# Performance work log

Hardware: AMD Instinct MI355X
Metric: run time of the kernel (lower is better)

The kernel has to match this reference:

```python
import jax, jax.numpy as jnp
import numpy as np


def _normalize(x):
    # channel mean-subtract then channel L2 normalize, as in MIDMs.forward
    x = x - x.mean(axis=1, keepdims=True)
    return x / jnp.linalg.norm(x, axis=1, keepdims=True)


def setup_inputs() -> dict:
    key = jax.random.key(0)
    ks = jax.random.split(key, 6)
    B, C, H, W = 2, 256, 64, 64
    return {
        "trg_out": jax.random.normal(ks[0], (B, C, H, W), jnp.float32),
        "src_out": jax.random.normal(ks[1], (B, C, H, W), jnp.float32),
        "ref_out": jax.random.normal(ks[2], (B, C, H, W), jnp.float32),
        "src_feats": jax.random.normal(ks[3], (B, 4, H, W), jnp.float32),
        "ref_feats": jax.random.normal(ks[4], (B, 4, H, W), jnp.float32),
        "ref_semantics": jax.random.uniform(ks[5], (B, 151, H, W), jnp.float32),
    }


def reference(trg_out, src_out, ref_out, src_feats, ref_feats, ref_semantics):
    B, C, H, W = trg_out.shape
    L = H * W
    # normalized matching features, flattened over spatial positions
    t = _normalize(trg_out).reshape(B, C, L)   # [B, C, Lt]
    s = _normalize(src_out).reshape(B, C, L)   # [B, C, Ls]
    r = _normalize(ref_out).reshape(B, C, L)

    # Correlation.correlation: dense cosine affinity between all position pairs
    corr_src = jnp.einsum("bci,bcj->bij", t, s)  # [B, Lt, Ls]
    corr_ref = jnp.einsum("bci,bcj->bij", t, r)

    # soft_warp: softmax over source positions, attention-weighted gather
    attn_src = jax.nn.softmax(corr_src, axis=-1)
    attn_ref = jax.nn.softmax(corr_ref, axis=-1)

    warped_src_feat = jnp.einsum("bij,bcj->bci", attn_src,
                                 src_feats.reshape(B, -1, L)).reshape(B, -1, H, W)
    warped_ref_feat = jnp.einsum("bij,bcj->bci", attn_ref,
                                 ref_feats.reshape(B, -1, L)).reshape(B, -1, H, W)
    warped_ref_seg = jnp.einsum("bij,bcj->bci", attn_ref,
                                ref_semantics.reshape(B, -1, L)).reshape(B, -1, H, W)
    return warped_src_feat, warped_ref_feat, warped_ref_seg
```

## Files before the change

kernel.cpp:

```cpp
#include <hip/hip_runtime.h>
#include <hip/hip_bf16.h>
#include <cstdint>
#include <cstddef>

typedef unsigned short u16;
typedef __attribute__((ext_vector_type(8))) __bf16 bf16x8;
typedef __attribute__((ext_vector_type(4))) unsigned u32x4;
typedef __attribute__((ext_vector_type(16))) float f32x16;

#define LPOS 4096
#define CDIM 256
#define LDSBUF 13312

#if __has_builtin(__builtin_amdgcn_exp2f)
#define EXP2(x) __builtin_amdgcn_exp2f(x)
#else
#define EXP2(x) exp2f(x)
#endif

#define GLOAD_LDS16(g, l)                                                      \
  __builtin_amdgcn_global_load_lds(                                            \
      (const __attribute__((address_space(1))) void*)(g),                      \
      (__attribute__((address_space(3))) void*)(l), 16, 0, 0)

__device__ __forceinline__ unsigned f2bfbits(float x) {
  union { float f; unsigned u; } v; v.f = x;
  return (v.u + 0x7FFFu + ((v.u >> 16) & 1u)) >> 16;
}
__device__ __forceinline__ unsigned packbf(float a, float b) {
  __hip_bfloat162 h2 = __float22bfloat162_rn(make_float2(a, b));
  return *(unsigned*)&h2;
}

__global__ void norm_fused(const float* __restrict__ t_in,
                           const float* __restrict__ s_in,
                           const float* __restrict__ r_in,
                           u16* __restrict__ qn, u16* __restrict__ ksn,
                           u16* __restrict__ krn) {
  __shared__ float tile[256 * 33];
  __shared__ float sums[256], sqs[256];
  __shared__ float mv[32], ivv[32];
  int idx = blockIdx.x;
  int ab = idx >> 7, lt = idx & 127;
  int arr = ab >> 1, b = ab & 1;
  int l0 = lt * 32;
  const float* inp = (arr == 0 ? t_in : arr == 1 ? s_in : r_in) + (size_t)b * CDIM * LPOS;
  u16* outp = (arr == 0 ? qn : arr == 1 ? ksn : krn) + (size_t)b * LPOS * CDIM;
  float scale = (arr == 0) ? 1.4426950408889634f : 1.0f;
  int t = threadIdx.x;
  int cg = t >> 5, l = t & 31;
  float sum = 0.f, sq = 0.f;
#pragma unroll 8
  for (int cc = 0; cc < 32; ++cc) {
    int c = cg * 32 + cc;
    float v = inp[(size_t)c * LPOS + l0 + l];
    tile[c * 33 + l] = v;
    sum += v; sq += v * v;
  }
  sums[t] = sum; sqs[t] = sq;
  __syncthreads();
  if (t < 32) {
    float s = 0.f, q = 0.f;
#pragma unroll
    for (int g = 0; g < 8; ++g) { s += sums[g * 32 + t]; q += sqs[g * 32 + t]; }
    float mean = s * (1.0f / CDIM);
    float nsq = q - s * s * (1.0f / CDIM);
    mv[t] = mean;
    ivv[t] = rsqrtf(fmaxf(nsq, 1e-20f)) * scale;
  }
  __syncthreads();
  int c2 = t & 127, ph = t >> 7;
#pragma unroll 4
  for (int rr = 0; rr < 16; ++rr) {
    int pos = ph + rr * 2;
    float m = mv[pos], iv = ivv[pos];
    float v0 = (tile[(2 * c2) * 33 + pos] - m) * iv;
    float v1 = (tile[(2 * c2 + 1) * 33 + pos] - m) * iv;
    *(unsigned*)&outp[(size_t)(l0 + pos) * CDIM + 2 * c2] = packbf(v0, v1);
  }
}

__global__ void build_v(const float* __restrict__ sf, const float* __restrict__ rf,
                        const float* __restrict__ sem,
                        u16* __restrict__ vs, u16* __restrict__ vr) {
  int t = blockIdx.x * 256 + threadIdx.x;
  const int NVS = 2 * 32 * 4096;
  if (t < NVS) {
    int b = t >> 17;
    int c = (t >> 12) & 31;
    int j = t & 4095;
    float v = (c < 4) ? sf[((size_t)b * 4 + c) * LPOS + j] : (c == 4 ? 1.0f : 0.0f);
    vs[t] = (u16)f2bfbits(v);
  } else {
    int t2 = t - NVS;
    if (t2 < 2 * 160 * 4096) {
      int b = t2 / (160 * 4096);
      int rr = t2 % (160 * 4096);
      int c = rr >> 12, j = rr & 4095;
      float v = (c < 151) ? sem[((size_t)b * 151 + c) * LPOS + j]
              : (c < 155) ? rf[((size_t)b * 4 + (c - 151)) * LPOS + j]
              : (c == 155) ? 1.0f : 0.0f;
      vr[((size_t)b * 160 + c) * LPOS + j] = (u16)f2bfbits(v);
    }
  }
}

template <int CT>
__device__ __forceinline__ void flash_body(
    const u16* __restrict__ qb, const u16* __restrict__ kb,
    const u16* __restrict__ vb, float* __restrict__ dst,
    u16 (*lds)[LDSBUF], int wave, int lane, int i_wave, int j_base, int iters) {
  int h = lane >> 5, ln = lane & 31;

  bf16x8 qf[16];
  const u16* qrow = qb + (size_t)(i_wave + ln) * CDIM;
#pragma unroll
  for (int kt = 0; kt < 16; ++kt)
    qf[kt] = *(const bf16x8*)(qrow + kt * 16 + h * 8);
#pragma unroll
  for (int kt = 0; kt < 16; ++kt)
    asm volatile("" : "+v"(*(u32x4*)&qf[kt]));

  f32x16 O[CT];
#pragma unroll
  for (int c = 0; c < CT; ++c)
#pragma unroll
    for (int t = 0; t < 16; ++t) O[c][t] = 0.0f;

  auto stage = [&](int j0s, int buf) {
#pragma unroll
    for (int g = 0; g < 4; ++g) {
      int G = wave * 4 + g;
      int j = 2 * G + h;
      GLOAD_LDS16(kb + (size_t)(j0s + j) * CDIM + (ln ^ (j & 7)) * 8,
                  &lds[buf][G * 512]);
    }
    if constexpr (CT == 5) {
#pragma unroll
      for (int g = 0; g < 3; ++g) {
        int s = wave + g * 4;
        if (s < 10) {
          int f = s * 64 + lane;
          int p = f / 160;
          int c = f - p * 160;
          GLOAD_LDS16(vb + (size_t)c * LPOS + j0s + p * 8,
                      &lds[buf][8192 + s * 512]);
        }
      }
    }
  };

  int kread_base = ln * 256 + 8 * (h ^ (ln & 1));
  int q = (ln >> 1) & 3;
  const u16* ka[4];
#pragma unroll
  for (int m = 0; m < 4; ++m) ka[m] = &lds[0][kread_base + 16 * (m ^ q)];
  const u16* va = &lds[0][8192 + h * 1280 + ln * 8];

  stage(j_base, 0);
  if (iters > 1) stage(j_base + 32, 1);

  int buf = 0;
  for (int jt = 0; jt < iters; ++jt) {
    int j0 = j_base + jt * 32;
    int bo = buf * LDSBUF;

    if (jt == iters - 1) {
      asm volatile("s_waitcnt vmcnt(0)" ::: "memory");
    } else if (CT == 5) {
      asm volatile("s_waitcnt vmcnt(6)" ::: "memory");
    } else {
      asm volatile("s_waitcnt vmcnt(4)" ::: "memory");
    }
    __builtin_amdgcn_sched_barrier(0);
    __builtin_amdgcn_s_barrier();
    __builtin_amdgcn_sched_barrier(0);

    bf16x8 vf[2];
    if constexpr (CT == 1) {
#pragma unroll
      for (int kt2 = 0; kt2 < 2; ++kt2)
        vf[kt2] = *(const bf16x8*)(vb + (size_t)ln * LPOS + j0 + (2 * kt2 + h) * 8);
    }
    if (jt + 2 < iters) {
      int b2 = buf ? buf - 1 : 2;
      stage(j0 + 64, b2);
    }

    __builtin_amdgcn_s_setprio(1);

    f32x16 Sa, Sb;
#pragma unroll
    for (int t = 0; t < 16; ++t) { Sa[t] = 0.0f; Sb[t] = 0.0f; }
#pragma unroll
    for (int kt = 0; kt < 16; kt += 2) {
      bf16x8 ka0 = *(const bf16x8*)(ka[kt & 3] + 64 * (kt >> 2) + bo);
      Sa = __builtin_amdgcn_mfma_f32_32x32x16_bf16(ka0, qf[kt], Sa, 0, 0, 0);
      bf16x8 ka1 = *(const bf16x8*)(ka[(kt + 1) & 3] + 64 * ((kt + 1) >> 2) + bo);
      Sb = __builtin_amdgcn_mfma_f32_32x32x16_bf16(ka1, qf[kt + 1], Sb, 0, 0, 0);
    }
    f32x16 S;
#pragma unroll
    for (int t = 0; t < 16; ++t) S[t] = EXP2(Sa[t] + Sb[t]);

    bf16x8 pb[2];
#pragma unroll
    for (int kh = 0; kh < 2; ++kh) {
      unsigned c0 = packbf(S[kh * 8 + 0], S[kh * 8 + 1]);
      unsigned c1 = packbf(S[kh * 8 + 2], S[kh * 8 + 3]);
      unsigned c2 = packbf(S[kh * 8 + 4], S[kh * 8 + 5]);
      unsigned c3 = packbf(S[kh * 8 + 6], S[kh * 8 + 7]);
      asm("v_permlane32_swap_b32 %0, %1" : "+v"(c0), "+v"(c2));
      asm("v_permlane32_swap_b32 %0, %1" : "+v"(c1), "+v"(c3));
      union { unsigned u[4]; bf16x8 v; } tmp;
      tmp.u[0] = c0;
      tmp.u[1] = c1;
      tmp.u[2] = c2;
      tmp.u[3] = c3;
      pb[kh] = tmp.v;
    }

#pragma unroll
    for (int ct = 0; ct < CT; ++ct)
#pragma unroll
      for (int kt2 = 0; kt2 < 2; ++kt2) {
        bf16x8 vax;
        if constexpr (CT == 5)
          vax = *(const bf16x8*)(va + kt2 * 2560 + ct * 256 + bo);
        else
          vax = vf[kt2];
        O[ct] = __builtin_amdgcn_mfma_f32_32x32x16_bf16(vax, pb[kt2], O[ct], 0, 0, 0);
      }

    __builtin_amdgcn_s_setprio(0);

    buf = (buf == 2) ? 0 : buf + 1;
  }

  const int climit = (CT == 1) ? 5 : 156;
#pragma unroll
  for (int ct = 0; ct < CT; ++ct)
#pragma unroll
    for (int t = 0; t < 16; ++t) {
      int c = ct * 32 + (t & 3) + 8 * (t >> 2) + 4 * h;
      if (c < climit)
        dst[(size_t)c * LPOS + i_wave + ln] = O[ct][t];
    }
}

__global__ __launch_bounds__(256, 2) void flash(
    const u16* __restrict__ qn, const u16* __restrict__ ksn, const u16* __restrict__ krn,
    const u16* __restrict__ vs, const u16* __restrict__ vr,
    float* __restrict__ nsrc, float* __restrict__ nref,
    int nch_src, int nch_ref) {
  __shared__ u16 lds[3][LDSBUF];
  int tid = threadIdx.x;
  int wave = tid >> 6, lane = tid & 63;
  int idx = blockIdx.x;
  int nrefb = 64 * nch_ref;
  if (idx < nrefb) {
    int r = idx;
    int chunk = r >> 6, b = (r >> 5) & 1, wgi = r & 31;
    int jchunk = LPOS / nch_ref;
    flash_body<5>(qn + (size_t)b * LPOS * CDIM, krn + (size_t)b * LPOS * CDIM,
                  vr + (size_t)b * 160 * LPOS,
                  nref + (size_t)(chunk * 2 + b) * 160 * LPOS,
                  lds, wave, lane, wgi * 128 + wave * 32, chunk * jchunk,
                  jchunk / 32);
  } else {
    int r = idx - nrefb;
    int chunk = r >> 6, b = (r >> 5) & 1, wgi = r & 31;
    int jchunk = LPOS / nch_src;
    flash_body<1>(qn + (size_t)b * LPOS * CDIM, ksn + (size_t)b * LPOS * CDIM,
                  vs + (size_t)b * 32 * LPOS,
                  nsrc + (size_t)(chunk * 2 + b) * 32 * LPOS,
                  lds, wave, lane, wgi * 128 + wave * 32, chunk * jchunk,
                  jchunk / 32);
  }
}

__global__ void finalize(const float* __restrict__ nsrc, const float* __restrict__ nref,
                         float* __restrict__ out, int nch_src, int nch_ref) {
  int v = blockIdx.x * 256 + threadIdx.x;
  if (v >= 325632) return;
  float nx = 0.f, ny = 0.f, nz = 0.f, nw = 0.f;
  float dx = 0.f, dy = 0.f, dz = 0.f, dw = 0.f;
  if (v < 8192) {
    int b = v >> 12, c = (v >> 10) & 3, i4 = v & 1023;
    for (int k = 0; k < nch_src; ++k) {
      const float* base = nsrc + ((size_t)(k * 2 + b) * 32) * LPOS;
      float4 n4 = ((const float4*)(base + (size_t)c * LPOS))[i4];
      float4 d4 = ((const float4*)(base + (size_t)4 * LPOS))[i4];
      nx += n4.x; ny += n4.y; nz += n4.z; nw += n4.w;
      dx += d4.x; dy += d4.y; dz += d4.z; dw += d4.w;
    }
  } else if (v < 16384) {
    int v1 = v - 8192;
    int b = v1 >> 12, c = (v1 >> 10) & 3, i4 = v1 & 1023;
    for (int k = 0; k < nch_ref; ++k) {
      const float* base = nref + ((size_t)(k * 2 + b) * 160) * LPOS;
      float4 n4 = ((const float4*)(base + (size_t)(151 + c) * LPOS))[i4];
      float4 d4 = ((const float4*)(base + (size_t)155 * LPOS))[i4];
      nx += n4.x; ny += n4.y; nz += n4.z; nw += n4.w;
      dx += d4.x; dy += d4.y; dz += d4.z; dw += d4.w;
    }
  } else {
    int v2 = v - 16384;
    int b = v2 / 154624;
    int rr = v2 - b * 154624;
    int c = rr >> 10, i4 = rr & 1023;
    for (int k = 0; k < nch_ref; ++k) {
      const float* base = nref + ((size_t)(k * 2 + b) * 160) * LPOS;
      float4 n4 = ((const float4*)(base + (size_t)c * LPOS))[i4];
      float4 d4 = ((const float4*)(base + (size_t)155 * LPOS))[i4];
      nx += n4.x; ny += n4.y; nz += n4.z; nw += n4.w;
      dx += d4.x; dy += d4.y; dz += d4.z; dw += d4.w;
    }
  }
  float4 r;
  r.x = nx / dx; r.y = ny / dy; r.z = nz / dz; r.w = nw / dw;
  ((float4*)out)[v] = r;
}

extern "C" void kernel_launch(void* const* d_in, const int* in_sizes, int n_in,
                              void* d_out, int out_size, void* d_ws, size_t ws_size,
                              hipStream_t stream) {
  const float* trg  = (const float*)d_in[0];
  const float* srcp = (const float*)d_in[1];
  const float* refp = (const float*)d_in[2];
  const float* sfeat = (const float*)d_in[3];
  const float* rfeat = (const float*)d_in[4];
  const float* rsem  = (const float*)d_in[5];
  float* out = (float*)d_out;

  char* ws = (char*)d_ws;
  size_t o = 0;
  auto alloc = [&](size_t bytes) -> char* {
    char* p = ws + o;
    o += (bytes + 255) & ~(size_t)255;
    return p;
  };
  u16* qn  = (u16*)alloc(2ull * LPOS * CDIM * 2);
  u16* ksn = (u16*)alloc(2ull * LPOS * CDIM * 2);
  u16* krn = (u16*)alloc(2ull * LPOS * CDIM * 2);
  u16* vs  = (u16*)alloc(2ull * 32 * LPOS * 2);
  u16* vr  = (u16*)alloc(2ull * 160 * LPOS * 2);

  size_t fixed = o;
  int nch_ref = 8;
  for (;;) {
    size_t need = fixed + 512 +
                  (size_t)nch_ref * 2 * 32 * LPOS * 4 +
                  (size_t)nch_ref * 2 * 160 * LPOS * 4;
    if (need <= ws_size || nch_ref == 1) break;
    nch_ref >>= 1;
  }
  int nch_src = nch_ref;
  float* nsrc = (float*)alloc((size_t)nch_src * 2 * 32 * LPOS * 4);
  float* nref = (float*)alloc((size_t)nch_ref * 2 * 160 * LPOS * 4);

  hipLaunchKernelGGL(norm_fused, dim3(768), dim3(256), 0, stream,
                     trg, srcp, refp, qn, ksn, krn);
  hipLaunchKernelGGL(build_v, dim3(6144), dim3(256), 0, stream,
                     sfeat, rfeat, rsem, vs, vr);
  hipLaunchKernelGGL(flash, dim3(64 * (nch_ref + nch_src)), dim3(256), 0, stream,
                     qn, ksn, krn, vs, vr, nsrc, nref, nch_src, nch_ref);
  hipLaunchKernelGGL(finalize, dim3(1272), dim3(256), 0, stream,
                     nsrc, nref, out, nch_src, nch_ref);
}
```

Baseline: 147.1 us.

## Software-pipeline QK MFMA with previous tile's exp and PV accumulation

Restructures the main loop so that each iteration computes the QK scores for the current tile, then runs exp, bf16 packing and the PV MFMAs for the previous tile, with a drain step after the loop. The goal is to hide the exp/transcendental latency and the dependency stalls between score and output MFMAs by interleaving independent work. It also drops the prefetch distance from two tiles ahead to one and waits for all outstanding loads (vmcnt(0)) each iteration, which may expose global load latency. The carried score accumulator adds register pressure.

```diff
diff --git a/kernel.cpp b/kernel.cpp
--- a/kernel.cpp
+++ b/kernel.cpp
@@ -157,52 +157,14 @@
   for (int m = 0; m < 4; ++m) ka[m] = &lds[0][kread_base + 16 * (m ^ q)];
   const u16* va = &lds[0][8192 + h * 1280 + ln * 8];
 
-  stage(j_base, 0);
-  if (iters > 1) stage(j_base + 32, 1);
-
-  int buf = 0;
-  for (int jt = 0; jt < iters; ++jt) {
-    int j0 = j_base + jt * 32;
-    int bo = buf * LDSBUF;
-
-    if (jt == iters - 1) {
-      asm volatile("s_waitcnt vmcnt(0)" ::: "memory");
-    } else if (CT == 5) {
-      asm volatile("s_waitcnt vmcnt(6)" ::: "memory");
-    } else {
-      asm volatile("s_waitcnt vmcnt(4)" ::: "memory");
-    }
-    __builtin_amdgcn_sched_barrier(0);
-    __builtin_amdgcn_s_barrier();
-    __builtin_amdgcn_sched_barrier(0);
-
-    bf16x8 vf[2];
-    if constexpr (CT == 1) {
-#pragma unroll
-      for (int kt2 = 0; kt2 < 2; ++kt2)
-        vf[kt2] = *(const bf16x8*)(vb + (size_t)ln * LPOS + j0 + (2 * kt2 + h) * 8);
-    }
-    if (jt + 2 < iters) {
-      int b2 = buf ? buf - 1 : 2;
-      stage(j0 + 64, b2);
-    }
-
-    __builtin_amdgcn_s_setprio(1);
-
-    f32x16 Sa, Sb;
-#pragma unroll
-    for (int t = 0; t < 16; ++t) { Sa[t] = 0.0f; Sb[t] = 0.0f; }
-#pragma unroll
-    for (int kt = 0; kt < 16; kt += 2) {
-      bf16x8 ka0 = *(const bf16x8*)(ka[kt & 3] + 64 * (kt >> 2) + bo);
-      Sa = __builtin_amdgcn_mfma_f32_32x32x16_bf16(ka0, qf[kt], Sa, 0, 0, 0);
-      bf16x8 ka1 = *(const bf16x8*)(ka[(kt + 1) & 3] + 64 * ((kt + 1) >> 2) + bo);
-      Sb = __builtin_amdgcn_mfma_f32_32x32x16_bf16(ka1, qf[kt + 1], Sb, 0, 0, 0);
-    }
+  f32x16 Sp;
+#pragma unroll
+  for (int t = 0; t < 16; ++t) Sp[t] = 0.0f;
+
+  auto finish_prev = [&](int pbo, const bf16x8* vfp) {
     f32x16 S;
 #pragma unroll
-    for (int t = 0; t < 16; ++t) S[t] = EXP2(Sa[t] + Sb[t]);
-
+    for (int t = 0; t < 16; ++t) S[t] = EXP2(Sp[t]);
     bf16x8 pb[2];
 #pragma unroll
     for (int kh = 0; kh < 2; ++kh) {
@@ -219,22 +181,75 @@
       tmp.u[3] = c3;
       pb[kh] = tmp.v;
     }
-
 #pragma unroll
     for (int ct = 0; ct < CT; ++ct)
 #pragma unroll
       for (int kt2 = 0; kt2 < 2; ++kt2) {
         bf16x8 vax;
         if constexpr (CT == 5)
-          vax = *(const bf16x8*)(va + kt2 * 2560 + ct * 256 + bo);
+          vax = *(const bf16x8*)(va + kt2 * 2560 + ct * 256 + pbo);
         else
-          vax = vf[kt2];
+          vax = vfp[kt2];
         O[ct] = __builtin_amdgcn_mfma_f32_32x32x16_bf16(vax, pb[kt2], O[ct], 0, 0, 0);
       }
+  };
+
+  stage(j_base, 0);
+
+  int buf = 0, pbo = 0;
+  for (int jt = 0; jt < iters; ++jt) {
+    int j0 = j_base + jt * 32;
+    int bo = buf * LDSBUF;
+
+    asm volatile("s_waitcnt vmcnt(0)" ::: "memory");
+    __builtin_amdgcn_sched_barrier(0);
+    __builtin_amdgcn_s_barrier();
+    __builtin_amdgcn_sched_barrier(0);
+
+    bf16x8 vf[2];
+    if (CT == 1 && jt >= 1) {
+#pragma unroll
+      for (int kt2 = 0; kt2 < 2; ++kt2)
+        vf[kt2] = *(const bf16x8*)(vb + (size_t)ln * LPOS + (j0 - 32) + (2 * kt2 + h) * 8);
+    }
+    if (jt + 1 < iters) {
+      int nb = (buf == 2) ? 0 : buf + 1;
+      stage(j0 + 32, nb);
+    }
+
+    __builtin_amdgcn_s_setprio(1);
+
+    f32x16 Sa, Sb;
+#pragma unroll
+    for (int t = 0; t < 16; ++t) { Sa[t] = 0.0f; Sb[t] = 0.0f; }
+#pragma unroll
+    for (int kt = 0; kt < 16; kt += 2) {
+      bf16x8 ka0 = *(const bf16x8*)(ka[kt & 3] + 64 * (kt >> 2) + bo);
+      Sa = __builtin_amdgcn_mfma_f32_32x32x16_bf16(ka0, qf[kt], Sa, 0, 0, 0);
+      bf16x8 ka1 = *(const bf16x8*)(ka[(kt + 1) & 3] + 64 * ((kt + 1) >> 2) + bo);
+      Sb = __builtin_amdgcn_mfma_f32_32x32x16_bf16(ka1, qf[kt + 1], Sb, 0, 0, 0);
+    }
+
+    if (jt >= 1) finish_prev(pbo, vf);
+
+#pragma unroll
+    for (int t = 0; t < 16; ++t) Sp[t] = Sa[t] + Sb[t];
 
     __builtin_amdgcn_s_setprio(0);
 
+    pbo = bo;
     buf = (buf == 2) ? 0 : buf + 1;
+  }
+
+  {
+    bf16x8 vf[2];
+    if constexpr (CT == 1) {
+      int jlast = j_base + (iters - 1) * 32;
+#pragma unroll
+      for (int kt2 = 0; kt2 < 2; ++kt2)
+        vf[kt2] = *(const bf16x8*)(vb + (size_t)ln * LPOS + jlast + (2 * kt2 + h) * 8);
+    }
+    finish_prev(pbo, vf);
   }
 
   const int climit = (CT == 1) ? 5 : 156;
```

Result: no change. 145.3 us (-1.2%).
